# Optimization experiments

Hardware: AMD Instinct MI355X
Metric: run time of the kernel (lower is better)

The kernel has to match this reference:

```python
import jax, jax.numpy as jnp
import numpy as np

EPS = 1e-5
BS, NA, NC, NL, NPTS, ED, NG = 1, 900, 6, 4, 13, 256, 8
GD = ED // NG
IMG_W, IMG_H = 704.0, 256.0
FMAP_HW = [(64, 176), (32, 88), (16, 44), (8, 22)]


def _ln(x, g, b):
    m = x.mean(-1, keepdims=True)
    v = ((x - m) ** 2).mean(-1, keepdims=True)
    return (x - m) / jnp.sqrt(v + EPS) * g + b


def _grid_sample(img, grid):
    # img: [N,C,H,W]; grid: [N,P,Q,2] in [-1,1]; bilinear, zeros padding, align_corners=False
    N, C, H, W = img.shape
    gx = jnp.clip((grid[..., 0] + 1.0) * (W * 0.5) - 0.5, -1e4, 1e4)
    gy = jnp.clip((grid[..., 1] + 1.0) * (H * 0.5) - 0.5, -1e4, 1e4)
    x0 = jnp.floor(gx); y0 = jnp.floor(gy)
    wx1 = gx - x0; wy1 = gy - y0; wx0 = 1.0 - wx1; wy0 = 1.0 - wy1
    x0i = x0.astype(jnp.int32); y0i = y0.astype(jnp.int32)
    flat = img.reshape(N, C, H * W)

    def corner(xi, yi, wgt):
        valid = (xi >= 0) & (xi < W) & (yi >= 0) & (yi < H)
        idx = (jnp.clip(yi, 0, H - 1) * W + jnp.clip(xi, 0, W - 1))
        g = jax.vmap(lambda f, i: f[:, i])(flat, idx.reshape(N, -1))  # [N,C,P*Q]
        g = g.reshape(N, C, idx.shape[1], idx.shape[2])
        return g * (wgt * valid)[:, None]

    return (corner(x0i, y0i, wx0 * wy0) + corner(x0i + 1, y0i, wx1 * wy0)
            + corner(x0i, y0i + 1, wx0 * wy1) + corner(x0i + 1, y0i + 1, wx1 * wy1))


def setup_inputs() -> dict:
    key = jax.random.key(0)
    ks = jax.random.split(key, 20)
    d = {}
    d['instance_feature'] = jax.random.normal(ks[0], (BS, NA, ED), jnp.float32)
    xyz = jax.random.normal(ks[1], (BS, NA, 3), jnp.float32) * 1.5
    size = jax.random.normal(ks[2], (BS, NA, 3), jnp.float32) * 0.3
    theta = jax.random.uniform(ks[3], (BS, NA, 1), jnp.float32) * (2.0 * np.pi)
    vel = jax.random.normal(ks[4], (BS, NA, 3), jnp.float32) * 0.1
    d['anchor'] = jnp.concatenate([xyz, size, jnp.sin(theta), jnp.cos(theta), vel], -1)
    d['anchor_embed'] = jax.random.normal(ks[5], (BS, NA, ED), jnp.float32)
    for i, (h, w) in enumerate(FMAP_HW):
        d[f'fmap{i}'] = jax.random.normal(ks[6 + i], (BS, NC, ED, h, w), jnp.float32)
    base = jnp.array([[80., 0., 0., 352.], [0., 80., 0., 128.],
                      [0., 0., 0., 1.], [0., 0., 0., 1.]], jnp.float32)
    proj = jnp.tile(base, (BS, NC, 1, 1))
    proj = proj.at[:, :, :2, :].add(jax.random.normal(ks[10], (BS, NC, 2, 4), jnp.float32) * 2.0)
    d['projection_mat'] = proj
    d['image_wh'] = jnp.broadcast_to(jnp.array([IMG_W, IMG_H], jnp.float32), (BS, NC, 2))
    d['fix_scale'] = jnp.array([[0, 0, 0], [0.45, 0, 0], [-0.45, 0, 0], [0, 0.45, 0],
                                [0, -0.45, 0], [0, 0, 0.45], [0, 0, -0.45]], jnp.float32)

    def w(k, shape):
        return jax.random.normal(k, shape, jnp.float32) * 0.02

    d['lfc_w'] = w(ks[11], (ED, 6 * 3)); d['lfc_b'] = jnp.zeros((18,), jnp.float32)
    d['cam_w1'] = w(ks[12], (12, ED)); d['cam_b1'] = jnp.zeros((ED,), jnp.float32)
    d['cam_g1'] = jnp.ones((ED,), jnp.float32); d['cam_be1'] = jnp.zeros((ED,), jnp.float32)
    d['cam_w2'] = w(ks[13], (ED, ED)); d['cam_b2'] = jnp.zeros((ED,), jnp.float32)
    d['cam_g2'] = jnp.ones((ED,), jnp.float32); d['cam_be2'] = jnp.zeros((ED,), jnp.float32)
    d['wfc_w'] = w(ks[14], (ED, NG * NL * NPTS)); d['wfc_b'] = jnp.zeros((NG * NL * NPTS,), jnp.float32)
    d['op_w'] = w(ks[15], (ED, ED)); d['op_b'] = jnp.zeros((ED,), jnp.float32)
    return d


def reference(instance_feature, anchor, anchor_embed, fmap0, fmap1, fmap2, fmap3,
              projection_mat, image_wh, fix_scale, lfc_w, lfc_b,
              cam_w1, cam_b1, cam_g1, cam_be1, cam_w2, cam_b2, cam_g2, cam_be2,
              wfc_w, wfc_b, op_w, op_b):
    bs, na = instance_feature.shape[:2]
    # ---- keypoint generation ----
    size = jnp.exp(anchor[..., None, 3:6])                       # [bs,na,1,3]
    kp = fix_scale * size                                        # [bs,na,7,3]
    ls = jax.nn.sigmoid(instance_feature @ lfc_w + lfc_b).reshape(bs, na, -1, 3) - 0.5
    kp = jnp.concatenate([kp, ls * size], axis=-2)               # [bs,na,NPTS,3]
    sin, cos = anchor[..., 6:7], anchor[..., 7:8]                # [bs,na,1]
    kx, ky, kz = kp[..., 0], kp[..., 1], kp[..., 2]
    key_points = jnp.stack([cos * kx - sin * ky, sin * kx + cos * ky, kz], -1) \
                 + anchor[..., None, 0:3]                        # [bs,na,NPTS,3]
    # ---- per-cam/level/point group weights ----
    feat = instance_feature + anchor_embed
    cam_in = projection_mat[:, :, :3].reshape(bs, NC, 12)
    h = jax.nn.relu(cam_in @ cam_w1 + cam_b1); h = _ln(h, cam_g1, cam_be1)
    h = jax.nn.relu(h @ cam_w2 + cam_b2); cam_embed = _ln(h, cam_g2, cam_be2)
    f = feat[:, :, None] + cam_embed[:, None]                    # [bs,na,NC,ED]
    wts = (f @ wfc_w + wfc_b).reshape(bs, na, NC * NL * NPTS, NG)
    wts = jax.nn.softmax(wts, axis=-2).reshape(bs, na, NC, NL, NPTS, NG)
    # ---- multi-cam projection + bilinear sampling ----
    pts = jnp.concatenate([key_points, jnp.ones_like(key_points[..., :1])], -1)
    p2d = jnp.einsum('bcij,banj->bcani', projection_mat, pts)    # [bs,NC,na,NPTS,4]
    p2d = p2d[..., :2] / jnp.maximum(p2d[..., 2:3], 1e-5)
    p2d = p2d / image_wh[:, :, None, None]
    grid = (p2d * 2.0 - 1.0).reshape(bs * NC, na, NPTS, 2)
    feats = jnp.stack([_grid_sample(fm.reshape(bs * NC, ED, fm.shape[-2], fm.shape[-1]), grid)
                       for fm in (fmap0, fmap1, fmap2, fmap3)], axis=1)  # [bs*NC,NL,ED,na,NPTS]
    feats = feats.reshape(bs, NC, NL, ED, na, NPTS).transpose(0, 4, 1, 2, 5, 3)  # [bs,na,NC,NL,NPTS,ED]
    # ---- group-weighted fusion over cams & levels, then sum over points ----
    fg = feats.reshape(bs, na, NC, NL, NPTS, NG, GD)
    fused = jnp.einsum('bnclpg,bnclpgd->bnpgd', wts, fg).reshape(bs, na, NPTS, ED)
    fused = fused.sum(axis=2)                                    # [bs,na,ED]
    out = fused @ op_w + op_b
    return jnp.concatenate([out, instance_feature], axis=-1)     # [bs,na,2*ED]
```

## Files before the change

### kernel.cpp

```cpp
#include <hip/hip_runtime.h>
#include <stdint.h>

#define NA 900
#define NC 6
#define NL 4
#define NPTS 13
#define ED 256
#define NG 8
#define LNEPS 1e-5f
#define NSTAGE 718303
#define NSTAGE_BLOCKS 2806
#define NTRANS 1416
#define NCOPY 672
#define NSAMP 312
#define LGS 313

struct PIn { const void* p[24]; };

__device__ __forceinline__ float b2f(unsigned short u){
  union { uint32_t i; float f; } v; v.i = ((uint32_t)u)<<16; return v.f;
}
__device__ __forceinline__ unsigned short f2b(float f){
  union { float f; uint32_t i; } v; v.f = f;
  uint32_t r = v.i + 0x7FFFu + ((v.i>>16)&1u);
  return (unsigned short)(r>>16);
}
#define BLO(u) __uint_as_float((u)<<16)
#define BHI(u) __uint_as_float((u)&0xffff0000u)

__device__ __forceinline__ float ldx(const void* p, int i, bool bf){
  return bf ? b2f(((const unsigned short*)p)[i]) : ((const float*)p)[i];
}

__device__ __forceinline__ bool sniff_bf(const unsigned short* __restrict__ u16){
  int lane = threadIdx.x & 63;
  unsigned short u = u16[2*lane];
  int e = (u>>7)&0xFF;
  int sane = (e>=110 && e<=135) ? 1 : 0;
  #pragma unroll
  for (int m=32;m;m>>=1) sane += __shfl_xor(sane, m);
  return sane >= 48;
}

__device__ __forceinline__ void blockReduce2(float& a, float& b, float* lds){
  #pragma unroll
  for (int m=32;m;m>>=1){ a += __shfl_xor(a,m); b += __shfl_xor(b,m); }
  int w = threadIdx.x>>6;
  if ((threadIdx.x&63)==0){ lds[w]=a; lds[w+4]=b; }
  __syncthreads();
  a = lds[0]+lds[1]+lds[2]+lds[3];
  b = lds[4]+lds[5]+lds[6]+lds[7];
  __syncthreads();
}

__global__ __launch_bounds__(256) void k_prep(PIn in, float* __restrict__ stage,
                                              unsigned short* __restrict__ tf,
                                              unsigned short* __restrict__ wfcw_h,
                                              unsigned short* __restrict__ opw_h,
                                              float* __restrict__ Bc){
  const bool bf = sniff_bf((const unsigned short*)in.p[0]);
  const int tid = threadIdx.x;
  int b = blockIdx.x;

  __shared__ unsigned short TT[2][64][64];
  __shared__ float h[ED];
  __shared__ float cE[ED];
  __shared__ float red8[8];
  __shared__ float part[4][64];

  if (b < NSTAGE_BLOCKS){
    const int cum[21] = {0,230400,240300,470700,470796,470808,470829,475437,475455,
                         478527,478783,479039,479295,544831,545087,545343,545599,
                         652095,652511,718047,718303};
    const int map[20] = {0,1,2,7,8,9,10,11,12,13,14,15,16,17,18,19,20,21,22,23};
    int idx = b*256 + tid;
    if (idx >= NSTAGE) return;
    int seg = 0, base = 0;
    #pragma unroll
    for (int s=1;s<20;s++) if (idx >= cum[s]){ seg = s; base = cum[s]; }
    const void* src = in.p[map[0]];
    #pragma unroll
    for (int s=1;s<20;s++) if (seg==s) src = in.p[map[s]];
    stage[idx] = ldx(src, idx - base, bf);
    return;
  }
  b -= NSTAGE_BLOCKS;
  if (b < NTRANS){
    const int tiles[4] = {44,11,3,1};
    const int HWs[4]   = {11264,2816,704,176};
    const int TFO[4]   = {0,17301504,21626880,22708224};
    int l, local;
    if      (b < 1056){ l=0; local=b;      }
    else if (b < 1320){ l=1; local=b-1056; }
    else if (b < 1392){ l=2; local=b-1320; }
    else              { l=3; local=b-1392; }
    int pt = local % tiles[l]; int rest = local / tiles[l];
    int ct = rest & 3; int c = rest >> 2;
    const int HW = HWs[l];
    const int px0 = pt*256;
    const void* src = in.p[3+l];
    const int j8 = tid & 7;
    const int w8 = tid >> 3;

    uint4 v[2][4];
    float4 cf[2][2];
    if (bf){
      #pragma unroll
      for (int p=0;p<2;p++){
        int ch = ct*64 + p*32 + w8;
        size_t rowb = (size_t)(c*ED+ch)*HW;
        #pragma unroll
        for (int q=0;q<4;q++){
          int pxs = px0 + q*64 + j8*8;
          v[p][q] = (pxs < HW)
            ? *reinterpret_cast<const uint4*>((const unsigned short*)src + rowb + pxs)
            : make_uint4(0,0,0,0);
        }
      }
    } else {
      #pragma unroll
      for (int p=0;p<2;p++){
        int ch = ct*64 + p*32 + w8;
        size_t rowb = (size_t)(c*ED+ch)*HW;
        int pxs = px0 + j8*8;
        if (pxs < HW){
          cf[p][0] = *reinterpret_cast<const float4*>((const float*)src + rowb + pxs);
          cf[p][1] = *reinterpret_cast<const float4*>((const float*)src + rowb + pxs + 4);
        } else { cf[p][0] = make_float4(0.f,0.f,0.f,0.f); cf[p][1] = cf[p][0]; }
      }
    }
    for (int q=0;q<4;q++){
      if (px0 + q*64 >= HW) break;
      uint4 wv[2];
      if (bf){
        wv[0] = v[0][q]; wv[1] = v[1][q];
      } else {
        #pragma unroll
        for (int p=0;p<2;p++){
          wv[p].x = (uint32_t)f2b(cf[p][0].x) | ((uint32_t)f2b(cf[p][0].y)<<16);
          wv[p].y = (uint32_t)f2b(cf[p][0].z) | ((uint32_t)f2b(cf[p][0].w)<<16);
          wv[p].z = (uint32_t)f2b(cf[p][1].x) | ((uint32_t)f2b(cf[p][1].y)<<16);
          wv[p].w = (uint32_t)f2b(cf[p][1].z) | ((uint32_t)f2b(cf[p][1].w)<<16);
        }
        if (q < 3 && px0 + (q+1)*64 < HW){
          #pragma unroll
          for (int p=0;p<2;p++){
            int ch = ct*64 + p*32 + w8;
            size_t rowb = (size_t)(c*ED+ch)*HW;
            int pxs = px0 + (q+1)*64 + j8*8;
            if (pxs < HW){
              cf[p][0] = *reinterpret_cast<const float4*>((const float*)src + rowb + pxs);
              cf[p][1] = *reinterpret_cast<const float4*>((const float*)src + rowb + pxs + 4);
            } else { cf[p][0] = make_float4(0.f,0.f,0.f,0.f); cf[p][1] = cf[p][0]; }
          }
        }
      }
      const int buf = q & 1;
      #pragma unroll
      for (int p=0;p<2;p++){
        int r = p*32 + w8;
        int g8 = (j8 ^ (r>>3))<<3;
        *reinterpret_cast<uint4*>(&TT[buf][r][g8]) = wv[p];
      }
      __syncthreads();
      #pragma unroll
      for (int p=0;p<2;p++){
        int pxl = p*32 + w8;
        int px  = px0 + q*64 + pxl;
        int colq = (((pxl>>3) ^ j8)<<3) | (pxl & 7);
        int rb = j8*8;
        unsigned short t0 = TT[buf][rb+0][colq], t1 = TT[buf][rb+1][colq];
        unsigned short t2 = TT[buf][rb+2][colq], t3 = TT[buf][rb+3][colq];
        unsigned short t4 = TT[buf][rb+4][colq], t5 = TT[buf][rb+5][colq];
        unsigned short t6 = TT[buf][rb+6][colq], t7 = TT[buf][rb+7][colq];
        uint4 o;
        o.x = (uint32_t)t0 | ((uint32_t)t1<<16);
        o.y = (uint32_t)t2 | ((uint32_t)t3<<16);
        o.z = (uint32_t)t4 | ((uint32_t)t5<<16);
        o.w = (uint32_t)t6 | ((uint32_t)t7<<16);
        if (px < HW)
          *reinterpret_cast<uint4*>(tf + TFO[l] + (size_t)c*HW*ED + (size_t)px*ED + ct*64 + j8*8) = o;
      }
    }
    return;
  }
  b -= NTRANS;
  if (b < NCOPY){
    int idx = b*256 + tid;
    if (idx < 106496){
      wfcw_h[idx] = bf ? ((const unsigned short*)in.p[20])[idx]
                       : f2b(((const float*)in.p[20])[idx]);
    } else {
      int j = idx - 106496;
      opw_h[j] = bf ? ((const unsigned short*)in.p[22])[j]
                    : f2b(((const float*)in.p[22])[j]);
    }
    return;
  }
  b -= NCOPY;
  {
    const void* proj = in.p[7];
    const void* w1 = in.p[12]; const void* b1 = in.p[13];
    const void* g1 = in.p[14]; const void* be1 = in.p[15];
    const void* w2 = in.p[16]; const void* b2 = in.p[17];
    const void* g2 = in.p[18]; const void* be2 = in.p[19];
    const void* wfcw = in.p[20]; const void* wfcb = in.p[21];
    const int c = b/7, colt = b - (b/7)*7;
    float ci[12];
    #pragma unroll
    for (int i=0;i<12;i++) ci[i] = ldx(proj, c*16+i, bf);
    float acc = ldx(b1, tid, bf);
    #pragma unroll
    for (int k=0;k<12;k++) acc += ci[k]*ldx(w1, k*ED+tid, bf);
    float x = fmaxf(acc, 0.f);
    float s=x, q=x*x;
    blockReduce2(s,q,red8);
    float mean = s*(1.f/ED), var = q*(1.f/ED)-mean*mean;
    h[tid] = (x-mean)*rsqrtf(var+LNEPS)*ldx(g1,tid,bf) + ldx(be1,tid,bf);
    __syncthreads();
    acc = ldx(b2, tid, bf);
    #pragma unroll 8
    for (int k=0;k<ED;k++) acc += h[k]*ldx(w2, k*ED+tid, bf);
    x = fmaxf(acc,0.f);
    s=x; q=x*x;
    blockReduce2(s,q,red8);
    mean = s*(1.f/ED); var = q*(1.f/ED)-mean*mean;
    cE[tid] = (x-mean)*rsqrtf(var+LNEPS)*ldx(g2,tid,bf) + ldx(be2,tid,bf);
    __syncthreads();
    const int kc = tid>>6, colL = tid&63, col = colt*64+colL;
    float a = 0.f;
    if (col < 416){
      #pragma unroll 8
      for (int k=0;k<64;k++) a += cE[kc*64+k]*ldx(wfcw, (kc*64+k)*416+col, bf);
    }
    part[kc][colL] = a;
    __syncthreads();
    if (kc==0 && col<416)
      Bc[c*416+col] = part[0][colL]+part[1][colL]+part[2][colL]+part[3][colL] + ldx(wfcb,col,bf);
  }
}

__global__ __launch_bounds__(512, 4) void k_anchor(
    const float* __restrict__ stage, const unsigned short* __restrict__ tf,
    const unsigned short* __restrict__ wfcw_h, const unsigned short* __restrict__ opw_h,
    const float* __restrict__ Bc, const void* __restrict__ rawinst,
    void* __restrict__ outv){
  const int n = blockIdx.x, tid = threadIdx.x;
  const bool bf = sniff_bf((const unsigned short*)rawinst);

  const float* s_inst = stage + 0;
  const float* s_anc  = stage + 230400;
  const float* s_ae   = stage + 240300;
  const float* s_proj = stage + 470700;
  const float* s_imwh = stage + 470796;
  const float* s_fixs = stage + 470808;
  const float* s_lw   = stage + 470829;
  const float* s_lb   = stage + 475437;
  const float* s_opb  = stage + 718047;

  __shared__ float ifs[ED];
  __shared__ float fe[ED];
  __shared__ float lg2[8*LGS];
  __shared__ uint4 cbi[NSAMP];
  __shared__ uint4 cwf[NSAMP];
  __shared__ unsigned short coff[NSAMP];
  __shared__ float red[8][ED+4];
  __shared__ float fu[ED];
  __shared__ float kp[13][3];
  __shared__ float sc[8];
  __shared__ float lsv[18];
  __shared__ int scnt;

  if (tid < 256){
    float iv = s_inst[n*ED+tid];
    ifs[tid] = iv;
    fe[tid]  = iv + s_ae[n*ED+tid];
  } else {
    int t = tid - 256;
    if (t == 0)      scnt = 0;
    if (t < 3)       sc[t] = s_anc[n*11+t];
    else if (t == 3) sc[3] = s_anc[n*11+6];
    else if (t == 4) sc[4] = s_anc[n*11+7];
    else if (t < 8)  sc[t] = __expf(s_anc[n*11+t-2]);
  }
  __syncthreads();
  if (tid < 144){
    int d = tid>>3, j = tid&7;
    float a = 0.f;
    #pragma unroll 8
    for (int k=j*32;k<j*32+32;k++) a += ifs[k]*s_lw[k*18+d];
    a += __shfl_xor(a,1); a += __shfl_xor(a,2); a += __shfl_xor(a,4);
    if (j==0){
      a += s_lb[d];
      lsv[d] = 1.f/(1.f+__expf(-a)) - 0.5f;
    }
  }
  __syncthreads();
  if (tid < 13){
    float kx,ky,kz;
    if (tid < 7){
      kx = s_fixs[tid*3+0]*sc[5];
      ky = s_fixs[tid*3+1]*sc[6];
      kz = s_fixs[tid*3+2]*sc[7];
    } else {
      int j = tid-7;
      kx = lsv[j*3+0]*sc[5]; ky = lsv[j*3+1]*sc[6]; kz = lsv[j*3+2]*sc[7];
    }
    kp[tid][0] = sc[4]*kx - sc[3]*ky + sc[0];
    kp[tid][1] = sc[3]*kx + sc[4]*ky + sc[1];
    kp[tid][2] = kz + sc[2];
  }
  if (tid < 416){
    float a0 = 0.f;
    #pragma unroll 8
    for (int k=0;k<ED;k++) a0 += fe[k]*b2f(wfcw_h[k*416+tid]);
    const int g = tid & 7, rr = tid >> 3;
    #pragma unroll
    for (int c=0;c<NC;c++)
      lg2[g*LGS + c*52 + rr] = a0 + Bc[c*416+tid];
  }
  __syncthreads();
  if (tid < NSAMP){
    int s = tid;
    int c = s/52, rr = s - c*52;
    int l = rr/13, p = rr - l*13;
    float m[12];
    #pragma unroll
    for (int i=0;i<12;i++) m[i] = s_proj[c*16+i];
    float X=kp[p][0], Y=kp[p][1], Z=kp[p][2];
    float x = m[0]*X + m[1]*Y + m[2]*Z  + m[3];
    float y = m[4]*X + m[5]*Y + m[6]*Z  + m[7];
    float z = m[8]*X + m[9]*Y + m[10]*Z + m[11];
    float d = fmaxf(z, 1e-5f);
    float px = x/(d*s_imwh[c*2+0]), py = y/(d*s_imwh[c*2+1]);
    const int W = 176>>l, H = 64>>l;
    const int TFO[4] = {0,17301504,21626880,22708224};
    float gx = fminf(fmaxf(px*(float)W - 0.5f, -10000.f), 10000.f);
    float gy = fminf(fmaxf(py*(float)H - 0.5f, -10000.f), 10000.f);
    float xf = floorf(gx), yf = floorf(gy);
    int x0 = (int)xf, y0 = (int)yf;
    float wx1 = gx-xf, wy1 = gy-yf;
    float wx0 = 1.f-wx1, wy0 = 1.f-wy1;
    bool vx0 = (x0>=0)&&(x0<W),   vx1 = (x0+1>=0)&&(x0+1<W);
    bool vy0 = (y0>=0)&&(y0<H),   vy1 = (y0+1>=0)&&(y0+1<H);
    float w00 = (vx0&&vy0) ? wx0*wy0 : 0.f;
    float w10 = (vx1&&vy0) ? wx1*wy0 : 0.f;
    float w01 = (vx0&&vy1) ? wx0*wy1 : 0.f;
    float w11 = (vx1&&vy1) ? wx1*wy1 : 0.f;
    if (w00+w10+w01+w11 != 0.f){
      int cx0 = min(max(x0,0),W-1), cx1 = min(max(x0+1,0),W-1);
      int cy0 = min(max(y0,0),H-1), cy1 = min(max(y0+1,0),H-1);
      uint32_t cam = (uint32_t)TFO[l] + (uint32_t)(c*H*W)*ED;
      uint4 bi, wv;
      bi.x = cam + (uint32_t)(cy0*W+cx0)*ED;
      bi.y = cam + (uint32_t)(cy0*W+cx1)*ED;
      bi.z = cam + (uint32_t)(cy1*W+cx0)*ED;
      bi.w = cam + (uint32_t)(cy1*W+cx1)*ED;
      wv.x = __float_as_uint(w00); wv.y = __float_as_uint(w10);
      wv.z = __float_as_uint(w01); wv.w = __float_as_uint(w11);
      int slot = atomicAdd(&scnt, 1);
      cbi[slot] = bi;
      cwf[slot] = wv;
      coff[slot] = (unsigned short)s;
    }
  }
  {
    const int g = tid>>6, j = tid&63;
    float v[5]; float mx = -1e30f;
    #pragma unroll
    for (int i=0;i<5;i++){
      int e = j + 64*i;
      float val = -1e30f;
      if (e < NSAMP){
        val = lg2[g*LGS + e];
        mx = fmaxf(mx, val);
      }
      v[i] = val;
    }
    #pragma unroll
    for (int mk=32;mk;mk>>=1) mx = fmaxf(mx, __shfl_xor(mx, mk));
    float sum = 0.f;
    #pragma unroll
    for (int i=0;i<5;i++){
      if (j + 64*i < NSAMP){ float ex = __expf(v[i]-mx); v[i] = ex; sum += ex; }
    }
    #pragma unroll
    for (int mk=32;mk;mk>>=1) sum += __shfl_xor(sum, mk);
    float inv = 1.f/sum;
    #pragma unroll
    for (int i=0;i<5;i++){
      int e = j + 64*i;
      if (e < NSAMP) lg2[g*LGS + e] = v[i]*inv;
    }
  }
  __syncthreads();
  {
    const int m = scnt;
    const int strm = tid>>5, lane32 = tid&31;
    const int ch8 = lane32*8, gg = lane32>>2;
    float acc[8] = {0,0,0,0,0,0,0,0};
    int i = strm;
    for (; i + 16 < m; i += 32){
      uint4 biA = cbi[i],    wfA = cwf[i];
      uint4 biB = cbi[i+16], wfB = cwf[i+16];
      float wgA = lg2[gg*LGS + coff[i]],  wgB = lg2[gg*LGS + coff[i+16]];
      uint4 a00 = *reinterpret_cast<const uint4*>(tf + biA.x + ch8);
      uint4 a10 = *reinterpret_cast<const uint4*>(tf + biA.y + ch8);
      uint4 a01 = *reinterpret_cast<const uint4*>(tf + biA.z + ch8);
      uint4 a11 = *reinterpret_cast<const uint4*>(tf + biA.w + ch8);
      uint4 b00 = *reinterpret_cast<const uint4*>(tf + biB.x + ch8);
      uint4 b10 = *reinterpret_cast<const uint4*>(tf + biB.y + ch8);
      uint4 b01 = *reinterpret_cast<const uint4*>(tf + biB.z + ch8);
      uint4 b11 = *reinterpret_cast<const uint4*>(tf + biB.w + ch8);
      float pA00 = wgA*__uint_as_float(wfA.x), pA10 = wgA*__uint_as_float(wfA.y);
      float pA01 = wgA*__uint_as_float(wfA.z), pA11 = wgA*__uint_as_float(wfA.w);
      float pB00 = wgB*__uint_as_float(wfB.x), pB10 = wgB*__uint_as_float(wfB.y);
      float pB01 = wgB*__uint_as_float(wfB.z), pB11 = wgB*__uint_as_float(wfB.w);
      acc[0] += pA00*BLO(a00.x)+pA10*BLO(a10.x)+pA01*BLO(a01.x)+pA11*BLO(a11.x)
              + pB00*BLO(b00.x)+pB10*BLO(b10.x)+pB01*BLO(b01.x)+pB11*BLO(b11.x);
      acc[1] += pA00*BHI(a00.x)+pA10*BHI(a10.x)+pA01*BHI(a01.x)+pA11*BHI(a11.x)
              + pB00*BHI(b00.x)+pB10*BHI(b10.x)+pB01*BHI(b01.x)+pB11*BHI(b11.x);
      acc[2] += pA00*BLO(a00.y)+pA10*BLO(a10.y)+pA01*BLO(a01.y)+pA11*BLO(a11.y)
              + pB00*BLO(b00.y)+pB10*BLO(b10.y)+pB01*BLO(b01.y)+pB11*BLO(b11.y);
      acc[3] += pA00*BHI(a00.y)+pA10*BHI(a10.y)+pA01*BHI(a01.y)+pA11*BHI(a11.y)
              + pB00*BHI(b00.y)+pB10*BHI(b10.y)+pB01*BHI(b01.y)+pB11*BHI(b11.y);
      acc[4] += pA00*BLO(a00.z)+pA10*BLO(a10.z)+pA01*BLO(a01.z)+pA11*BLO(a11.z)
              + pB00*BLO(b00.z)+pB10*BLO(b10.z)+pB01*BLO(b01.z)+pB11*BLO(b11.z);
      acc[5] += pA00*BHI(a00.z)+pA10*BHI(a10.z)+pA01*BHI(a01.z)+pA11*BHI(a11.z)
              + pB00*BHI(b00.z)+pB10*BHI(b10.z)+pB01*BHI(b01.z)+pB11*BHI(b11.z);
      acc[6] += pA00*BLO(a00.w)+pA10*BLO(a10.w)+pA01*BLO(a01.w)+pA11*BLO(a11.w)
              + pB00*BLO(b00.w)+pB10*BLO(b10.w)+pB01*BLO(b01.w)+pB11*BLO(b11.w);
      acc[7] += pA00*BHI(a00.w)+pA10*BHI(a10.w)+pA01*BHI(a01.w)+pA11*BHI(a11.w)
              + pB00*BHI(b00.w)+pB10*BHI(b10.w)+pB01*BHI(b01.w)+pB11*BHI(b11.w);
    }
    for (; i < m; i += 16){
      uint4 bi = cbi[i], wf = cwf[i];
      float wg = lg2[gg*LGS + coff[i]];
      uint4 q00 = *reinterpret_cast<const uint4*>(tf + bi.x + ch8);
      uint4 q10 = *reinterpret_cast<const uint4*>(tf + bi.y + ch8);
      uint4 q01 = *reinterpret_cast<const uint4*>(tf + bi.z + ch8);
      uint4 q11 = *reinterpret_cast<const uint4*>(tf + bi.w + ch8);
      float p00 = wg*__uint_as_float(wf.x), p10 = wg*__uint_as_float(wf.y);
      float p01 = wg*__uint_as_float(wf.z), p11 = wg*__uint_as_float(wf.w);
      acc[0] += p00*BLO(q00.x)+p10*BLO(q10.x)+p01*BLO(q01.x)+p11*BLO(q11.x);
      acc[1] += p00*BHI(q00.x)+p10*BHI(q10.x)+p01*BHI(q01.x)+p11*BHI(q11.x);
      acc[2] += p00*BLO(q00.y)+p10*BLO(q10.y)+p01*BLO(q01.y)+p11*BLO(q11.y);
      acc[3] += p00*BHI(q00.y)+p10*BHI(q10.y)+p01*BHI(q01.y)+p11*BHI(q11.y);
      acc[4] += p00*BLO(q00.z)+p10*BLO(q10.z)+p01*BLO(q01.z)+p11*BLO(q11.z);
      acc[5] += p00*BHI(q00.z)+p10*BHI(q10.z)+p01*BHI(q01.z)+p11*BHI(q11.z);
      acc[6] += p00*BLO(q00.w)+p10*BLO(q10.w)+p01*BLO(q01.w)+p11*BLO(q11.w);
      acc[7] += p00*BHI(q00.w)+p10*BHI(q10.w)+p01*BHI(q01.w)+p11*BHI(q11.w);
    }
    #pragma unroll
    for (int j=0;j<8;j++) acc[j] += __shfl_xor(acc[j], 32);
    const int w = tid>>6;
    if ((tid&63) < 32){
      *reinterpret_cast<float4*>(&red[w][ch8])   = make_float4(acc[0],acc[1],acc[2],acc[3]);
      *reinterpret_cast<float4*>(&red[w][ch8+4]) = make_float4(acc[4],acc[5],acc[6],acc[7]);
    }
  }
  __syncthreads();
  if (tid < 256){
    float r = 0.f;
    #pragma unroll
    for (int i=0;i<8;i++) r += red[i][tid];
    fu[tid] = r;
  }
  __syncthreads();
  {
    const int col = tid & 255, half = tid >> 8;
    const int k0 = half*128;
    float a = 0.f;
    #pragma unroll 8
    for (int k=k0;k<k0+128;k++) a += fu[k]*b2f(opw_h[k*ED+col]);
    red[half][col] = a;
  }
  __syncthreads();
  {
    float v;
    if (tid < 256) v = s_opb[tid] + red[0][tid] + red[1][tid];
    else           v = ifs[tid-256];
    if (bf) ((unsigned short*)outv)[n*512+tid] = f2b(v);
    else    ((float*)outv)[n*512+tid]          = v;
  }
}

extern "C" void kernel_launch(void* const* d_in, const int* in_sizes, int n_in,
                              void* d_out, int out_size, void* d_ws, size_t ws_size,
                              hipStream_t stream){
  char* ws = (char*)d_ws;
  size_t off = 0;
  auto alloc = [&](size_t bytes)->char*{
    char* p = ws + off; off += (bytes + 63) & ~size_t(63); return p;
  };
  unsigned short* tf = (unsigned short*)alloc((size_t)22978560*2);
  float* stage  = (float*)alloc((size_t)NSTAGE*4);
  unsigned short* wfcw_h = (unsigned short*)alloc((size_t)106496*2);
  unsigned short* opw_h  = (unsigned short*)alloc((size_t)65536*2);
  float* Bc     = (float*)alloc((size_t)NC*416*4);

  PIn in;
  for (int i=0;i<24;i++) in.p[i] = d_in[i];

  k_prep<<<NSTAGE_BLOCKS + NTRANS + NCOPY + 42, 256, 0, stream>>>(in, stage, tf, wfcw_h, opw_h, Bc);
  k_anchor<<<NA, 512, 0, stream>>>(stage, tf, wfcw_h, opw_h, Bc, d_in[0], d_out);
}
```

Measured before the change: 253.5 us.

## Split anchor kernel so per-anchor sampling setup overlaps feature-map transpose

The pipeline is restructured into three kernels. The small staging, weight-copy and camera-embedding blocks now run first. The feature-map transpose blocks then share a launch with a new per-anchor setup phase: the weight-logit GEMV, softmax and projection/bilinear descriptor generation, which writes compact descriptors (indices, bilinear weights, per-group softmax weights) to global memory. A final gather kernel loads these descriptors into LDS and does the bilinear accumulation and output projection. The aim is to overlap the anchor setup work with the bandwidth-bound transpose and to shrink the gather kernel's LDS and prologue. The cost is an extra launch and about 18 MB of descriptor traffic through global memory.

```diff
diff --git a/kernel.cpp b/kernel.cpp
--- a/kernel.cpp
+++ b/kernel.cpp
@@ -53,8 +53,7 @@
   __syncthreads();
 }
 
-__global__ __launch_bounds__(256) void k_prep(PIn in, float* __restrict__ stage,
-                                              unsigned short* __restrict__ tf,
+__global__ __launch_bounds__(256) void k_init(PIn in, float* __restrict__ stage,
                                               unsigned short* __restrict__ wfcw_h,
                                               unsigned short* __restrict__ opw_h,
                                               float* __restrict__ Bc){
@@ -62,7 +61,6 @@
   const int tid = threadIdx.x;
   int b = blockIdx.x;
 
-  __shared__ unsigned short TT[2][64][64];
   __shared__ float h[ED];
   __shared__ float cE[ED];
   __shared__ float red8[8];
@@ -85,6 +83,80 @@
     return;
   }
   b -= NSTAGE_BLOCKS;
+  if (b < NCOPY){
+    int idx = b*256 + tid;
+    if (idx < 106496){
+      wfcw_h[idx] = bf ? ((const unsigned short*)in.p[20])[idx]
+                       : f2b(((const float*)in.p[20])[idx]);
+    } else {
+      int j = idx - 106496;
+      opw_h[j] = bf ? ((const unsigned short*)in.p[22])[j]
+                    : f2b(((const float*)in.p[22])[j]);
+    }
+    return;
+  }
+  b -= NCOPY;
+  {
+    const void* proj = in.p[7];
+    const void* w1 = in.p[12]; const void* b1 = in.p[13];
+    const void* g1 = in.p[14]; const void* be1 = in.p[15];
+    const void* w2 = in.p[16]; const void* b2 = in.p[17];
+    const void* g2 = in.p[18]; const void* be2 = in.p[19];
+    const void* wfcw = in.p[20]; const void* wfcb = in.p[21];
+    const int c = b/7, colt = b - (b/7)*7;
+    float ci[12];
+    #pragma unroll
+    for (int i=0;i<12;i++) ci[i] = ldx(proj, c*16+i, bf);
+    float acc = ldx(b1, tid, bf);
+    #pragma unroll
+    for (int k=0;k<12;k++) acc += ci[k]*ldx(w1, k*ED+tid, bf);
+    float x = fmaxf(acc, 0.f);
+    float s=x, q=x*x;
+    blockReduce2(s,q,red8);
+    float mean = s*(1.f/ED), var = q*(1.f/ED)-mean*mean;
+    h[tid] = (x-mean)*rsqrtf(var+LNEPS)*ldx(g1,tid,bf) + ldx(be1,tid,bf);
+    __syncthreads();
+    acc = ldx(b2, tid, bf);
+    #pragma unroll 8
+    for (int k=0;k<ED;k++) acc += h[k]*ldx(w2, k*ED+tid, bf);
+    x = fmaxf(acc,0.f);
+    s=x; q=x*x;
+    blockReduce2(s,q,red8);
+    mean = s*(1.f/ED); var = q*(1.f/ED)-mean*mean;
+    cE[tid] = (x-mean)*rsqrtf(var+LNEPS)*ldx(g2,tid,bf) + ldx(be2,tid,bf);
+    __syncthreads();
+    const int kc = tid>>6, colL = tid&63, col = colt*64+colL;
+    float a = 0.f;
+    if (col < 416){
+      #pragma unroll 8
+      for (int k=0;k<64;k++) a += cE[kc*64+k]*ldx(wfcw, (kc*64+k)*416+col, bf);
+    }
+    part[kc][colL] = a;
+    __syncthreads();
+    if (kc==0 && col<416)
+      Bc[c*416+col] = part[0][colL]+part[1][colL]+part[2][colL]+part[3][colL] + ldx(wfcb,col,bf);
+  }
+}
+
+__global__ __launch_bounds__(256) void k_work(PIn in, const float* __restrict__ stage,
+                                              unsigned short* __restrict__ tf,
+                                              const unsigned short* __restrict__ wfcw_h,
+                                              const float* __restrict__ Bc,
+                                              uint4* __restrict__ gdesc, int* __restrict__ mcnt,
+                                              void* __restrict__ outv){
+  const bool bf = sniff_bf((const unsigned short*)in.p[0]);
+  const int tid = threadIdx.x;
+  int b = blockIdx.x;
+
+  __shared__ unsigned short TT[2][64][64];
+  __shared__ float ifs[ED];
+  __shared__ float fe[ED];
+  __shared__ float lg2[8*LGS];
+  __shared__ float kp[13][3];
+  __shared__ float sc[8];
+  __shared__ float lsv[18];
+  __shared__ int scnt;
+
   if (b < NTRANS){
     const int tiles[4] = {44,11,3,1};
     const int HWs[4]   = {11264,2816,704,176};
@@ -184,70 +256,7 @@
     }
     return;
   }
-  b -= NTRANS;
-  if (b < NCOPY){
-    int idx = b*256 + tid;
-    if (idx < 106496){
-      wfcw_h[idx] = bf ? ((const unsigned short*)in.p[20])[idx]
-                       : f2b(((const float*)in.p[20])[idx]);
-    } else {
-      int j = idx - 106496;
-      opw_h[j] = bf ? ((const unsigned short*)in.p[22])[j]
-                    : f2b(((const float*)in.p[22])[j]);
-    }
-    return;
-  }
-  b -= NCOPY;
-  {
-    const void* proj = in.p[7];
-    const void* w1 = in.p[12]; const void* b1 = in.p[13];
-    const void* g1 = in.p[14]; const void* be1 = in.p[15];
-    const void* w2 = in.p[16]; const void* b2 = in.p[17];
-    const void* g2 = in.p[18]; const void* be2 = in.p[19];
-    const void* wfcw = in.p[20]; const void* wfcb = in.p[21];
-    const int c = b/7, colt = b - (b/7)*7;
-    float ci[12];
-    #pragma unroll
-    for (int i=0;i<12;i++) ci[i] = ldx(proj, c*16+i, bf);
-    float acc = ldx(b1, tid, bf);
-    #pragma unroll
-    for (int k=0;k<12;k++) acc += ci[k]*ldx(w1, k*ED+tid, bf);
-    float x = fmaxf(acc, 0.f);
-    float s=x, q=x*x;
-    blockReduce2(s,q,red8);
-    float mean = s*(1.f/ED), var = q*(1.f/ED)-mean*mean;
-    h[tid] = (x-mean)*rsqrtf(var+LNEPS)*ldx(g1,tid,bf) + ldx(be1,tid,bf);
-    __syncthreads();
-    acc = ldx(b2, tid, bf);
-    #pragma unroll 8
-    for (int k=0;k<ED;k++) acc += h[k]*ldx(w2, k*ED+tid, bf);
-    x = fmaxf(acc,0.f);
-    s=x; q=x*x;
-    blockReduce2(s,q,red8);
-    mean = s*(1.f/ED); var = q*(1.f/ED)-mean*mean;
-    cE[tid] = (x-mean)*rsqrtf(var+LNEPS)*ldx(g2,tid,bf) + ldx(be2,tid,bf);
-    __syncthreads();
-    const int kc = tid>>6, colL = tid&63, col = colt*64+colL;
-    float a = 0.f;
-    if (col < 416){
-      #pragma unroll 8
-      for (int k=0;k<64;k++) a += cE[kc*64+k]*ldx(wfcw, (kc*64+k)*416+col, bf);
-    }
-    part[kc][colL] = a;
-    __syncthreads();
-    if (kc==0 && col<416)
-      Bc[c*416+col] = part[0][colL]+part[1][colL]+part[2][colL]+part[3][colL] + ldx(wfcb,col,bf);
-  }
-}
-
-__global__ __launch_bounds__(512, 4) void k_anchor(
-    const float* __restrict__ stage, const unsigned short* __restrict__ tf,
-    const unsigned short* __restrict__ wfcw_h, const unsigned short* __restrict__ opw_h,
-    const float* __restrict__ Bc, const void* __restrict__ rawinst,
-    void* __restrict__ outv){
-  const int n = blockIdx.x, tid = threadIdx.x;
-  const bool bf = sniff_bf((const unsigned short*)rawinst);
-
+  const int n = b - NTRANS;
   const float* s_inst = stage + 0;
   const float* s_anc  = stage + 230400;
   const float* s_ae   = stage + 240300;
@@ -256,32 +265,21 @@
   const float* s_fixs = stage + 470808;
   const float* s_lw   = stage + 470829;
   const float* s_lb   = stage + 475437;
-  const float* s_opb  = stage + 718047;
-
-  __shared__ float ifs[ED];
-  __shared__ float fe[ED];
-  __shared__ float lg2[8*LGS];
-  __shared__ uint4 cbi[NSAMP];
-  __shared__ uint4 cwf[NSAMP];
-  __shared__ unsigned short coff[NSAMP];
-  __shared__ float red[8][ED+4];
-  __shared__ float fu[ED];
-  __shared__ float kp[13][3];
-  __shared__ float sc[8];
-  __shared__ float lsv[18];
-  __shared__ int scnt;
-
-  if (tid < 256){
+
+  {
+    if (tid==0) scnt = 0;
     float iv = s_inst[n*ED+tid];
     ifs[tid] = iv;
     fe[tid]  = iv + s_ae[n*ED+tid];
-  } else {
-    int t = tid - 256;
-    if (t == 0)      scnt = 0;
-    if (t < 3)       sc[t] = s_anc[n*11+t];
-    else if (t == 3) sc[3] = s_anc[n*11+6];
-    else if (t == 4) sc[4] = s_anc[n*11+7];
-    else if (t < 8)  sc[t] = __expf(s_anc[n*11+t-2]);
+    if (bf) ((unsigned short*)outv)[n*512+256+tid] = f2b(iv);
+    else    ((float*)outv)[n*512+256+tid]          = iv;
+    if (tid >= 256-8){
+      int t = tid - (256-8);
+      if (t < 3)       sc[t] = s_anc[n*11+t];
+      else if (t == 3) sc[3] = s_anc[n*11+6];
+      else if (t == 4) sc[4] = s_anc[n*11+7];
+      else             sc[t] = __expf(s_anc[n*11+t-2]);
+    }
   }
   __syncthreads();
   if (tid < 144){
@@ -310,100 +308,136 @@
     kp[tid][1] = sc[3]*kx + sc[4]*ky + sc[1];
     kp[tid][2] = kz + sc[2];
   }
-  if (tid < 416){
-    float a0 = 0.f;
-    #pragma unroll 8
-    for (int k=0;k<ED;k++) a0 += fe[k]*b2f(wfcw_h[k*416+tid]);
+  {
+    int col2 = (tid < 160) ? tid+256 : 415;
+    float a0 = 0.f, a1 = 0.f;
+    #pragma unroll 4
+    for (int k=0;k<ED;k++){
+      float fv = fe[k];
+      a0 += fv*b2f(wfcw_h[k*416+tid]);
+      a1 += fv*b2f(wfcw_h[k*416+col2]);
+    }
     const int g = tid & 7, rr = tid >> 3;
-    #pragma unroll
-    for (int c=0;c<NC;c++)
+    const int g2 = col2 & 7, rr2 = col2 >> 3;
+    #pragma unroll
+    for (int c=0;c<NC;c++){
       lg2[g*LGS + c*52 + rr] = a0 + Bc[c*416+tid];
-  }
-  __syncthreads();
-  if (tid < NSAMP){
-    int s = tid;
-    int c = s/52, rr = s - c*52;
-    int l = rr/13, p = rr - l*13;
-    float m[12];
-    #pragma unroll
-    for (int i=0;i<12;i++) m[i] = s_proj[c*16+i];
-    float X=kp[p][0], Y=kp[p][1], Z=kp[p][2];
-    float x = m[0]*X + m[1]*Y + m[2]*Z  + m[3];
-    float y = m[4]*X + m[5]*Y + m[6]*Z  + m[7];
-    float z = m[8]*X + m[9]*Y + m[10]*Z + m[11];
-    float d = fmaxf(z, 1e-5f);
-    float px = x/(d*s_imwh[c*2+0]), py = y/(d*s_imwh[c*2+1]);
-    const int W = 176>>l, H = 64>>l;
-    const int TFO[4] = {0,17301504,21626880,22708224};
-    float gx = fminf(fmaxf(px*(float)W - 0.5f, -10000.f), 10000.f);
-    float gy = fminf(fmaxf(py*(float)H - 0.5f, -10000.f), 10000.f);
-    float xf = floorf(gx), yf = floorf(gy);
-    int x0 = (int)xf, y0 = (int)yf;
-    float wx1 = gx-xf, wy1 = gy-yf;
-    float wx0 = 1.f-wx1, wy0 = 1.f-wy1;
-    bool vx0 = (x0>=0)&&(x0<W),   vx1 = (x0+1>=0)&&(x0+1<W);
-    bool vy0 = (y0>=0)&&(y0<H),   vy1 = (y0+1>=0)&&(y0+1<H);
-    float w00 = (vx0&&vy0) ? wx0*wy0 : 0.f;
-    float w10 = (vx1&&vy0) ? wx1*wy0 : 0.f;
-    float w01 = (vx0&&vy1) ? wx0*wy1 : 0.f;
-    float w11 = (vx1&&vy1) ? wx1*wy1 : 0.f;
-    if (w00+w10+w01+w11 != 0.f){
-      int cx0 = min(max(x0,0),W-1), cx1 = min(max(x0+1,0),W-1);
-      int cy0 = min(max(y0,0),H-1), cy1 = min(max(y0+1,0),H-1);
-      uint32_t cam = (uint32_t)TFO[l] + (uint32_t)(c*H*W)*ED;
-      uint4 bi, wv;
-      bi.x = cam + (uint32_t)(cy0*W+cx0)*ED;
-      bi.y = cam + (uint32_t)(cy0*W+cx1)*ED;
-      bi.z = cam + (uint32_t)(cy1*W+cx0)*ED;
-      bi.w = cam + (uint32_t)(cy1*W+cx1)*ED;
-      wv.x = __float_as_uint(w00); wv.y = __float_as_uint(w10);
-      wv.z = __float_as_uint(w01); wv.w = __float_as_uint(w11);
-      int slot = atomicAdd(&scnt, 1);
-      cbi[slot] = bi;
-      cwf[slot] = wv;
-      coff[slot] = (unsigned short)s;
-    }
-  }
-  {
-    const int g = tid>>6, j = tid&63;
-    float v[5]; float mx = -1e30f;
-    #pragma unroll
-    for (int i=0;i<5;i++){
-      int e = j + 64*i;
+      if (tid < 160) lg2[g2*LGS + c*52 + rr2] = a1 + Bc[c*416+col2];
+    }
+  }
+  __syncthreads();
+  {
+    const int g = tid>>5, j = tid&31;
+    float v[10]; float mx = -1e30f;
+    #pragma unroll
+    for (int i=0;i<10;i++){
+      int e = j + 32*i;
       float val = -1e30f;
-      if (e < NSAMP){
-        val = lg2[g*LGS + e];
-        mx = fmaxf(mx, val);
+      if (e < NSAMP){ val = lg2[g*LGS + e]; mx = fmaxf(mx, val); }
+      v[i] = val;
+    }
+    #pragma unroll
+    for (int mk=16;mk;mk>>=1) mx = fmaxf(mx, __shfl_xor(mx, mk, 32));
+    float sum = 0.f;
+    #pragma unroll
+    for (int i=0;i<10;i++){
+      if (j + 32*i < NSAMP){ float ex = __expf(v[i]-mx); v[i] = ex; sum += ex; }
+    }
+    #pragma unroll
+    for (int mk=16;mk;mk>>=1) sum += __shfl_xor(sum, mk, 32);
+    float inv = 1.f/sum;
+    #pragma unroll
+    for (int i=0;i<10;i++){
+      int e = j + 32*i;
+      if (e < NSAMP) lg2[g*LGS + e] = v[i]*inv;
+    }
+  }
+  __syncthreads();
+  #pragma unroll
+  for (int pass=0;pass<2;pass++){
+    int s = tid + pass*256;
+    if (s < NSAMP){
+      int c = s/52, rr = s - c*52;
+      int l = rr/13, p = rr - l*13;
+      float m[12];
+      #pragma unroll
+      for (int i=0;i<12;i++) m[i] = s_proj[c*16+i];
+      float X=kp[p][0], Y=kp[p][1], Z=kp[p][2];
+      float x = m[0]*X + m[1]*Y + m[2]*Z  + m[3];
+      float y = m[4]*X + m[5]*Y + m[6]*Z  + m[7];
+      float z = m[8]*X + m[9]*Y + m[10]*Z + m[11];
+      float d = fmaxf(z, 1e-5f);
+      float px = x/(d*s_imwh[c*2+0]), py = y/(d*s_imwh[c*2+1]);
+      const int W = 176>>l, H = 64>>l;
+      const int TFO[4] = {0,17301504,21626880,22708224};
+      float gx = fminf(fmaxf(px*(float)W - 0.5f, -10000.f), 10000.f);
+      float gy = fminf(fmaxf(py*(float)H - 0.5f, -10000.f), 10000.f);
+      float xf = floorf(gx), yf = floorf(gy);
+      int x0 = (int)xf, y0 = (int)yf;
+      float wx1 = gx-xf, wy1 = gy-yf;
+      float wx0 = 1.f-wx1, wy0 = 1.f-wy1;
+      bool vx0 = (x0>=0)&&(x0<W),   vx1 = (x0+1>=0)&&(x0+1<W);
+      bool vy0 = (y0>=0)&&(y0<H),   vy1 = (y0+1>=0)&&(y0+1<H);
+      float w00 = (vx0&&vy0) ? wx0*wy0 : 0.f;
+      float w10 = (vx1&&vy0) ? wx1*wy0 : 0.f;
+      float w01 = (vx0&&vy1) ? wx0*wy1 : 0.f;
+      float w11 = (vx1&&vy1) ? wx1*wy1 : 0.f;
+      if (w00+w10+w01+w11 != 0.f){
+        int cx0 = min(max(x0,0),W-1), cx1 = min(max(x0+1,0),W-1);
+        int cy0 = min(max(y0,0),H-1), cy1 = min(max(y0+1,0),H-1);
+        uint32_t cam = (uint32_t)TFO[l] + (uint32_t)(c*H*W)*ED;
+        uint4 bi, wv;
+        bi.x = cam + (uint32_t)(cy0*W+cx0)*ED;
+        bi.y = cam + (uint32_t)(cy0*W+cx1)*ED;
+        bi.z = cam + (uint32_t)(cy1*W+cx0)*ED;
+        bi.w = cam + (uint32_t)(cy1*W+cx1)*ED;
+        wv.x = __float_as_uint(w00); wv.y = __float_as_uint(w10);
+        wv.z = __float_as_uint(w01); wv.w = __float_as_uint(w11);
+        float4 wa = make_float4(lg2[0*LGS+s], lg2[1*LGS+s], lg2[2*LGS+s], lg2[3*LGS+s]);
+        float4 wb = make_float4(lg2[4*LGS+s], lg2[5*LGS+s], lg2[6*LGS+s], lg2[7*LGS+s]);
+        int slot = atomicAdd(&scnt, 1);
+        uint4* dst = gdesc + (size_t)(n*NSAMP + slot)*4;
+        dst[0] = bi;
+        dst[1] = wv;
+        dst[2] = *reinterpret_cast<uint4*>(&wa);
+        dst[3] = *reinterpret_cast<uint4*>(&wb);
       }
-      v[i] = val;
-    }
-    #pragma unroll
-    for (int mk=32;mk;mk>>=1) mx = fmaxf(mx, __shfl_xor(mx, mk));
-    float sum = 0.f;
-    #pragma unroll
-    for (int i=0;i<5;i++){
-      if (j + 64*i < NSAMP){ float ex = __expf(v[i]-mx); v[i] = ex; sum += ex; }
-    }
-    #pragma unroll
-    for (int mk=32;mk;mk>>=1) sum += __shfl_xor(sum, mk);
-    float inv = 1.f/sum;
-    #pragma unroll
-    for (int i=0;i<5;i++){
-      int e = j + 64*i;
-      if (e < NSAMP) lg2[g*LGS + e] = v[i]*inv;
-    }
-  }
-  __syncthreads();
-  {
-    const int m = scnt;
+    }
+  }
+  __syncthreads();
+  if (tid==0) mcnt[n] = scnt;
+}
+
+__global__ __launch_bounds__(512, 4) void k_gather(
+    const float* __restrict__ stage, const unsigned short* __restrict__ tf,
+    const unsigned short* __restrict__ opw_h, const uint4* __restrict__ gdesc,
+    const int* __restrict__ mcnt, const void* __restrict__ rawinst,
+    void* __restrict__ outv){
+  const int n = blockIdx.x, tid = threadIdx.x;
+  const bool bf = sniff_bf((const unsigned short*)rawinst);
+  const float* s_opb = stage + 718047;
+
+  __shared__ uint4 ldesc[NSAMP*4];
+  __shared__ float red[8][ED+4];
+  __shared__ float fu[ED];
+
+  const int m = mcnt[n];
+  {
+    const uint4* src = gdesc + (size_t)n*NSAMP*4;
+    for (int j=tid; j < m*4; j += 512) ldesc[j] = src[j];
+  }
+  __syncthreads();
+
+  {
     const int strm = tid>>5, lane32 = tid&31;
     const int ch8 = lane32*8, gg = lane32>>2;
     float acc[8] = {0,0,0,0,0,0,0,0};
     int i = strm;
     for (; i + 16 < m; i += 32){
-      uint4 biA = cbi[i],    wfA = cwf[i];
-      uint4 biB = cbi[i+16], wfB = cwf[i+16];
-      float wgA = lg2[gg*LGS + coff[i]],  wgB = lg2[gg*LGS + coff[i+16]];
+      uint4 biA = ldesc[i*4],      wfA = ldesc[i*4+1];
+      uint4 biB = ldesc[(i+16)*4], wfB = ldesc[(i+16)*4+1];
+      float wgA = reinterpret_cast<const float*>(&ldesc[i*4+2])[gg];
+      float wgB = reinterpret_cast<const float*>(&ldesc[(i+16)*4+2])[gg];
       uint4 a00 = *reinterpret_cast<const uint4*>(tf + biA.x + ch8);
       uint4 a10 = *reinterpret_cast<const uint4*>(tf + biA.y + ch8);
       uint4 a01 = *reinterpret_cast<const uint4*>(tf + biA.z + ch8);
@@ -434,8 +468,8 @@
               + pB00*BHI(b00.w)+pB10*BHI(b10.w)+pB01*BHI(b01.w)+pB11*BHI(b11.w);
     }
     for (; i < m; i += 16){
-      uint4 bi = cbi[i], wf = cwf[i];
-      float wg = lg2[gg*LGS + coff[i]];
+      uint4 bi = ldesc[i*4], wf = ldesc[i*4+1];
+      float wg = reinterpret_cast<const float*>(&ldesc[i*4+2])[gg];
       uint4 q00 = *reinterpret_cast<const uint4*>(tf + bi.x + ch8);
       uint4 q10 = *reinterpret_cast<const uint4*>(tf + bi.y + ch8);
       uint4 q01 = *reinterpret_cast<const uint4*>(tf + bi.z + ch8);
@@ -476,10 +510,8 @@
     red[half][col] = a;
   }
   __syncthreads();
-  {
-    float v;
-    if (tid < 256) v = s_opb[tid] + red[0][tid] + red[1][tid];
-    else           v = ifs[tid-256];
+  if (tid < 256){
+    float v = s_opb[tid] + red[0][tid] + red[1][tid];
     if (bf) ((unsigned short*)outv)[n*512+tid] = f2b(v);
     else    ((float*)outv)[n*512+tid]          = v;
   }
@@ -498,10 +530,13 @@
   unsigned short* wfcw_h = (unsigned short*)alloc((size_t)106496*2);
   unsigned short* opw_h  = (unsigned short*)alloc((size_t)65536*2);
   float* Bc     = (float*)alloc((size_t)NC*416*4);
+  uint4* gdesc  = (uint4*)alloc((size_t)NA*NSAMP*64);
+  int*   mcnt   = (int*)alloc((size_t)NA*4);
 
   PIn in;
   for (int i=0;i<24;i++) in.p[i] = d_in[i];
 
-  k_prep<<<NSTAGE_BLOCKS + NTRANS + NCOPY + 42, 256, 0, stream>>>(in, stage, tf, wfcw_h, opw_h, Bc);
-  k_anchor<<<NA, 512, 0, stream>>>(stage, tf, wfcw_h, opw_h, Bc, d_in[0], d_out);
-}
+  k_init<<<NSTAGE_BLOCKS + NCOPY + 42, 256, 0, stream>>>(in, stage, wfcw_h, opw_h, Bc);
+  k_work<<<NTRANS + NA, 256, 0, stream>>>(in, stage, tf, wfcw_h, Bc, gdesc, mcnt, d_out);
+  k_gather<<<NA, 512, 0, stream>>>(stage, tf, opw_h, gdesc, mcnt, d_in[0], d_out);
+}
```

Measured after the change: 265.3 us. 4.6% more time.
